# Kernel optimization log

Hardware: AMD Instinct MI355X
Metric: run time of the kernel (lower is better)

## Reference

```python
import jax, jax.numpy as jnp
import numpy as np

B, T, C = 4, 1024, 1024
N_HEAD = 16
MEMORY = 64  # sliding-window size: key j visible to query i iff 0 <= i-j <= MEMORY


def setup_inputs() -> dict:
    key = jax.random.key(0)
    k1, k2, k3 = jax.random.split(key, 3)
    x = jax.random.normal(k1, (B, T, C), dtype=jnp.float32)
    # torch Linear weight is [out, in]; we store transposed [in, out] for x @ W
    W_attn = jax.random.normal(k2, (C, 3 * C), dtype=jnp.float32) * (1.0 / np.sqrt(C))
    W_proj = jax.random.normal(k3, (C, C), dtype=jnp.float32) * (1.0 / np.sqrt(C))
    return {"x": x, "W_attn": W_attn, "W_proj": W_proj}


def reference(x, W_attn, W_proj):
    Bv, Tv, Cv = x.shape
    hd = Cv // N_HEAD
    qkv = x @ W_attn                               # [B,T,3C]
    q, k, v = jnp.split(qkv, 3, axis=-1)
    def heads(t):
        return t.reshape(Bv, Tv, N_HEAD, hd).transpose(0, 2, 1, 3)  # [B,H,T,hd]
    q, k, v = heads(q), heads(k), heads(v)
    scale = 1.0 / np.sqrt(hd)
    scores = jnp.einsum('bhqd,bhkd->bhqk', q, k) * scale            # [B,H,T,T]
    i = jnp.arange(Tv)
    diff = i[:, None] - i[None, :]                                  # i - j
    band_mask = (diff >= 0) & (diff <= MEMORY)                      # M1 * ~M2
    y = jax.nn.softmax(jnp.where(band_mask, scores, -jnp.inf), axis=-1) @ v
    # get_att=True path: full causal attention probabilities (no window)
    att = jax.nn.softmax(jnp.where(diff >= 0, scores, -jnp.inf), axis=-1)
    att_std = jnp.std(att, axis=0, ddof=1)                          # torch .std default ddof=1
    y = y.transpose(0, 2, 1, 3).reshape(Bv, Tv, Cv)
    y = y @ W_proj
    return (y, att, att_std)
```

## Files before the change

### kernel.cpp

```cpp
#include <hip/hip_runtime.h>
#include <hip/hip_bf16.h>
#include <stdint.h>

#define Bb 4
#define Tt 1024
#define Hh 16
#define HD 64
#define C3 3072
#define WIN 64

typedef __bf16 bf16x8 __attribute__((ext_vector_type(8)));
typedef float f32x4 __attribute__((ext_vector_type(4)));

#define MFMA16(a, b, c) __builtin_amdgcn_mfma_f32_16x16x32_bf16((a), (b), (c), 0, 0, 0)

static __device__ __forceinline__ unsigned short f2bf(float f) {
  union { float f; unsigned u; } v; v.f = f;
  unsigned r = (v.u + 0x7FFFu + ((v.u >> 16) & 1u)) >> 16;
  return (unsigned short)r;
}
static __device__ __forceinline__ float bf2f(unsigned short h) {
  union { unsigned u; float f; } v; v.u = ((unsigned)h) << 16;
  return v.f;
}

__global__ __launch_bounds__(256) void k_prep(const float* __restrict__ x,
                                              const float* __restrict__ Wa,
                                              const float* __restrict__ Wp,
                                              unsigned short* __restrict__ xbf,
                                              unsigned short* __restrict__ WtA,
                                              unsigned short* __restrict__ WtP) {
  __shared__ float tile[32][33];
  const int blk = blockIdx.x;
  const int tid = threadIdx.x;
  if (blk < 4096) {
    int i = blk * 256 + tid;
    float4 v = ((const float4*)x)[i];
    ushort4 o;
    o.x = f2bf(v.x); o.y = f2bf(v.y); o.z = f2bf(v.z); o.w = f2bf(v.w);
    ((ushort4*)xbf)[i] = o;
    return;
  }
  const float* Win; unsigned short* Wt; int N, n0, k0;
  if (blk < 7168) { int bb = blk - 4096; Win = Wa; Wt = WtA; N = 3072; n0 = (bb % 96) * 32; k0 = (bb / 96) * 32; }
  else           { int bb = blk - 7168; Win = Wp; Wt = WtP; N = 1024; n0 = (bb % 32) * 32; k0 = (bb / 32) * 32; }
  const int K = 1024;
  int tx = tid & 31, ty = tid >> 5;
  for (int r = ty; r < 32; r += 8)
    tile[r][tx] = Win[(size_t)(k0 + r) * N + n0 + tx];
  __syncthreads();
  for (int r = ty; r < 32; r += 8)
    Wt[(size_t)(n0 + r) * K + k0 + tx] = f2bf(tile[tx][r]);
}

template <int BF16_OUT, int SCALEQ>
__global__ __launch_bounds__(256) void k_gemm_bt(const unsigned short* __restrict__ A,
                                                 const unsigned short* __restrict__ Bt,
                                                 void* __restrict__ Cv, int M, int N, int K) {
  __shared__ unsigned short lds[2 * 128 * 32];
  unsigned short* as_ = lds;
  unsigned short* bs_ = lds + 128 * 32;
  const int tid = threadIdx.x;
  const int m0 = blockIdx.x * 128, n0 = blockIdx.y * 128;
  const int w = tid >> 6, lane = tid & 63;
  const int wm = (w >> 1) * 64, wn = (w & 1) * 64;
  const int lrow = lane & 15, lk = lane >> 4;

  f32x4 z = {0.f, 0.f, 0.f, 0.f};
  f32x4 acc[4][4];
#pragma unroll
  for (int i = 0; i < 4; ++i)
#pragma unroll
    for (int j = 0; j < 4; ++j) acc[i][j] = z;

  const int nk = K >> 5;
  for (int kt = 0; kt < nk; ++kt) {
    const int k0 = kt << 5;
    __syncthreads();
#pragma unroll
    for (int p = 0; p < 2; ++p) {
      int seg = tid + p * 256;
      int row = seg >> 2, ks = (seg & 3) << 3;
      __builtin_amdgcn_global_load_lds(
          (__attribute__((address_space(1))) void*)(A + (size_t)(m0 + row) * K + k0 + ks),
          (__attribute__((address_space(3))) void*)(as_ + seg * 8), 16, 0, 0);
      __builtin_amdgcn_global_load_lds(
          (__attribute__((address_space(1))) void*)(Bt + (size_t)(n0 + row) * K + k0 + ks),
          (__attribute__((address_space(3))) void*)(bs_ + seg * 8), 16, 0, 0);
    }
    __syncthreads();
    bf16x8 af[4], bfr[4];
#pragma unroll
    for (int f = 0; f < 4; ++f) {
      af[f] = *(const bf16x8*)(as_ + (wm + f * 16 + lrow) * 32 + lk * 8);
      bfr[f] = *(const bf16x8*)(bs_ + (wn + f * 16 + lrow) * 32 + lk * 8);
    }
#pragma unroll
    for (int i = 0; i < 4; ++i)
#pragma unroll
      for (int j = 0; j < 4; ++j) acc[i][j] = MFMA16(af[i], bfr[j], acc[i][j]);
  }
  const int r0 = lk * 4;
#pragma unroll
  for (int i = 0; i < 4; ++i)
#pragma unroll
    for (int j = 0; j < 4; ++j)
#pragma unroll
      for (int r = 0; r < 4; ++r) {
        int gm = m0 + wm + i * 16 + r0 + r;
        int gn = n0 + wn + j * 16 + lrow;
        float v = acc[i][j][r];
        if (SCALEQ) {
          if (gn < 1024) v *= 0.125f;
        }
        if (BF16_OUT)
          ((unsigned short*)Cv)[(size_t)gm * N + gn] = f2bf(v);
        else
          ((float*)Cv)[(size_t)gm * N + gn] = v;
      }
}

__global__ __launch_bounds__(256) void k_att(const unsigned short* __restrict__ qkv,
                                             float* __restrict__ att, float* __restrict__ astd) {
  const int ti = 31 - blockIdx.x;
  const int h = blockIdx.y;
  const int i0 = ti * 32;
  const int tid = threadIdx.x;
  const int w = tid >> 6, lane = tid & 63;
  const int lrow = lane & 15, lk = lane >> 4;

  __shared__ float smr[4][32][2];
  __shared__ float wbuf[4][32][36];

  {
    const int b1 = w;
    const size_t qb_ = ((size_t)(b1 * Tt + i0 + lrow)) * C3 + h * 64 + lk * 8;
    bf16x8 q00 = *(const bf16x8*)(qkv + qb_);
    bf16x8 q01 = *(const bf16x8*)(qkv + qb_ + 32);
    bf16x8 q10 = *(const bf16x8*)(qkv + qb_ + (size_t)16 * C3);
    bf16x8 q11 = *(const bf16x8*)(qkv + qb_ + (size_t)16 * C3 + 32);

    float m[2][4], l[2][4];
#pragma unroll
    for (int i2 = 0; i2 < 2; ++i2)
#pragma unroll
      for (int r = 0; r < 4; ++r) { m[i2][r] = -1e30f; l[i2][r] = 0.f; }

    for (int jt = 0; jt <= ti; ++jt) {
      const int j0 = jt * 32;
      const size_t krowa = ((size_t)(b1 * Tt + j0 + lrow)) * C3 + 1024 + h * 64 + lk * 8;
      const size_t krowb = krowa + (size_t)16 * C3;
      bf16x8 k00 = *(const bf16x8*)(qkv + krowa);
      bf16x8 k01 = *(const bf16x8*)(qkv + krowa + 32);
      bf16x8 k10 = *(const bf16x8*)(qkv + krowb);
      bf16x8 k11 = *(const bf16x8*)(qkv + krowb + 32);
      const int ja = j0 + lrow, jb2 = j0 + 16 + lrow;
#pragma unroll
      for (int i2 = 0; i2 < 2; ++i2) {
        bf16x8 qa = i2 ? q10 : q00;
        bf16x8 qb = i2 ? q11 : q01;
        f32x4 sa = {0.f, 0.f, 0.f, 0.f}, sb = {0.f, 0.f, 0.f, 0.f};
        sa = MFMA16(qa, k00, sa);
        sa = MFMA16(qb, k01, sa);
        sb = MFMA16(qa, k10, sb);
        sb = MFMA16(qb, k11, sb);
#pragma unroll
        for (int r = 0; r < 4; ++r) {
          int ig = i0 + i2 * 16 + lk * 4 + r;
          int oka = (ja <= ig), okb = (jb2 <= ig);
          float va = oka ? sa[r] : -1e30f;
          float vb = okb ? sb[r] : -1e30f;
          float mn = fmaxf(m[i2][r], fmaxf(va, vb));
          float pa = oka ? __expf(sa[r] - mn) : 0.f;
          float pb = okb ? __expf(sb[r] - mn) : 0.f;
          l[i2][r] = l[i2][r] * __expf(m[i2][r] - mn) + pa + pb;
          m[i2][r] = mn;
        }
      }
    }
#pragma unroll
    for (int i2 = 0; i2 < 2; ++i2)
#pragma unroll
      for (int r = 0; r < 4; ++r) {
        float mm = m[i2][r], ll = l[i2][r];
#pragma unroll
        for (int d = 1; d <= 8; d <<= 1) {
          float mo = __shfl_xor(mm, d);
          float lo = __shfl_xor(ll, d);
          float mn = fmaxf(mm, mo);
          ll = ll * __expf(mm - mn) + lo * __expf(mo - mn);
          mm = mn;
        }
        if (lrow == 0) {
          int row = i2 * 16 + lk * 4 + r;
          smr[b1][row][0] = mm;
          smr[b1][row][1] = 1.0f / ll;
        }
      }
  }
  __syncthreads();

  bf16x8 qf[4][2][2];
#pragma unroll
  for (int b = 0; b < 4; ++b) {
    const size_t qb_ = ((size_t)(b * Tt + i0 + lrow)) * C3 + h * 64 + lk * 8;
    qf[b][0][0] = *(const bf16x8*)(qkv + qb_);
    qf[b][0][1] = *(const bf16x8*)(qkv + qb_ + 32);
    qf[b][1][0] = *(const bf16x8*)(qkv + qb_ + (size_t)16 * C3);
    qf[b][1][1] = *(const bf16x8*)(qkv + qb_ + (size_t)16 * C3 + 32);
  }

  const float4 z4 = make_float4(0.f, 0.f, 0.f, 0.f);
  for (int jt = w; jt < 32; jt += 4) {
    const int j0 = jt * 32;
    if (jt > ti) {
#pragma unroll
      for (int b = 0; b < 4; ++b)
#pragma unroll
        for (int q = 0; q < 4; ++q) {
          int f = q * 64 + lane;
          int row = f >> 3, c4 = f & 7;
          *(float4*)&att[(((size_t)(b * Hh + h)) * Tt + i0 + row) * Tt + j0 + c4 * 4] = z4;
        }
#pragma unroll
      for (int q = 0; q < 4; ++q) {
        int f = q * 64 + lane;
        int row = f >> 3, c4 = f & 7;
        *(float4*)&astd[((size_t)h * Tt + i0 + row) * Tt + j0 + c4 * 4] = z4;
      }
      continue;
    }
    float s1[2][2][4], s2[2][2][4];
#pragma unroll
    for (int i2 = 0; i2 < 2; ++i2)
#pragma unroll
      for (int j2 = 0; j2 < 2; ++j2)
#pragma unroll
        for (int r = 0; r < 4; ++r) { s1[i2][j2][r] = 0.f; s2[i2][j2][r] = 0.f; }

#pragma unroll
    for (int b = 0; b < 4; ++b) {
      const size_t krowa = ((size_t)(b * Tt + j0 + lrow)) * C3 + 1024 + h * 64 + lk * 8;
      const size_t krowb = krowa + (size_t)16 * C3;
      bf16x8 k00 = *(const bf16x8*)(qkv + krowa);
      bf16x8 k01 = *(const bf16x8*)(qkv + krowa + 32);
      bf16x8 k10 = *(const bf16x8*)(qkv + krowb);
      bf16x8 k11 = *(const bf16x8*)(qkv + krowb + 32);
#pragma unroll
      for (int i2 = 0; i2 < 2; ++i2) {
        float mm[4], rr[4];
#pragma unroll
        for (int r = 0; r < 4; ++r) {
          int row = i2 * 16 + lk * 4 + r;
          mm[r] = smr[b][row][0];
          rr[r] = smr[b][row][1];
        }
#pragma unroll
        for (int j2 = 0; j2 < 2; ++j2) {
          f32x4 s = {0.f, 0.f, 0.f, 0.f};
          s = MFMA16(qf[b][i2][0], j2 ? k10 : k00, s);
          s = MFMA16(qf[b][i2][1], j2 ? k11 : k01, s);
          const int jg = j0 + j2 * 16 + lrow;
#pragma unroll
          for (int r = 0; r < 4; ++r) {
            int ig = i0 + i2 * 16 + lk * 4 + r;
            float p = (jg <= ig) ? __expf(s[r] - mm[r]) * rr[r] : 0.f;
            wbuf[w][i2 * 16 + lk * 4 + r][j2 * 16 + lrow] = p;
            s1[i2][j2][r] += p;
            s2[i2][j2][r] += p * p;
          }
        }
      }
#pragma unroll
      for (int q = 0; q < 4; ++q) {
        int f = q * 64 + lane;
        int row = f >> 3, c4 = f & 7;
        float4 v = *(float4*)&wbuf[w][row][c4 * 4];
        *(float4*)&att[(((size_t)(b * Hh + h)) * Tt + i0 + row) * Tt + j0 + c4 * 4] = v;
      }
    }
#pragma unroll
    for (int i2 = 0; i2 < 2; ++i2)
#pragma unroll
      for (int j2 = 0; j2 < 2; ++j2)
#pragma unroll
        for (int r = 0; r < 4; ++r) {
          float mean = s1[i2][j2][r] * 0.25f;
          float var = (s2[i2][j2][r] - 4.f * mean * mean) * (1.f / 3.f);
          wbuf[w][i2 * 16 + lk * 4 + r][j2 * 16 + lrow] = sqrtf(fmaxf(var, 0.f));
        }
#pragma unroll
    for (int q = 0; q < 4; ++q) {
      int f = q * 64 + lane;
      int row = f >> 3, c4 = f & 7;
      float4 v = *(float4*)&wbuf[w][row][c4 * 4];
      *(float4*)&astd[((size_t)h * Tt + i0 + row) * Tt + j0 + c4 * 4] = v;
    }
  }
}

__global__ __launch_bounds__(256) void k_bandy(const unsigned short* __restrict__ qkv,
                                               unsigned short* __restrict__ yh) {
  __shared__ unsigned short qls[64 * 66];
  __shared__ unsigned short kls[128 * 66];
  __shared__ unsigned short vls[128 * 66];
  __shared__ float pls[4][80];

  int blk = blockIdx.x;
  int it = blk & 15, h = (blk >> 4) & 15, b = blk >> 8;
  int i0 = it * 64;
  int jb = i0 - 64;
  int tid = threadIdx.x;

  for (int r = tid; r < 320; r += 256) {
    unsigned short* dst;
    int grow, sel;
    if (r < 64) { dst = qls + r * 66; grow = i0 + r; sel = 0; }
    else if (r < 192) { dst = kls + (r - 64) * 66; grow = jb + (r - 64); sel = 1; }
    else { dst = vls + (r - 192) * 66; grow = jb + (r - 192); sel = 2; }
    if (grow < 0) {
      for (int t = 0; t < 32; ++t) ((unsigned*)dst)[t] = 0u;
    } else {
      const unsigned* src = (const unsigned*)(qkv + ((size_t)(b * Tt + grow)) * C3 + sel * 1024 + h * 64);
      for (int t = 0; t < 32; ++t) ((unsigned*)dst)[t] = src[t];
    }
  }
  __syncthreads();

  const int w = tid >> 6, lane = tid & 63;
  for (int rr = 0; rr < 16; ++rr) {
    const int i = i0 + (w << 4) + rr;
    const int io = i - i0;
    const int ja = i - 64 + lane;
    const unsigned* qrow = (const unsigned*)(qls + io * 66);
    const unsigned* krow = (const unsigned*)(kls + (size_t)(io + lane) * 66);
    const unsigned* kerow = (const unsigned*)(kls + (size_t)(io + 64) * 66);
    float sa = 0.f, se = 0.f;
#pragma unroll 8
    for (int t = 0; t < 32; ++t) {
      unsigned qq = qrow[t];
      float q0 = bf2f((unsigned short)qq), q1 = bf2f((unsigned short)(qq >> 16));
      unsigned kk = krow[t];
      sa = fmaf(q0, bf2f((unsigned short)kk), sa);
      sa = fmaf(q1, bf2f((unsigned short)(kk >> 16)), sa);
      unsigned ke = kerow[t];
      se = fmaf(q0, bf2f((unsigned short)ke), se);
      se = fmaf(q1, bf2f((unsigned short)(ke >> 16)), se);
    }
    if (ja < 0) sa = -1e30f;
    float m = sa;
    m = fmaxf(m, __shfl_xor(m, 1));
    m = fmaxf(m, __shfl_xor(m, 2));
    m = fmaxf(m, __shfl_xor(m, 4));
    m = fmaxf(m, __shfl_xor(m, 8));
    m = fmaxf(m, __shfl_xor(m, 16));
    m = fmaxf(m, __shfl_xor(m, 32));
    m = fmaxf(m, se);
    float pa = __expf(sa - m);
    float pe = __expf(se - m);
    float sum = pa;
    sum += __shfl_xor(sum, 1);
    sum += __shfl_xor(sum, 2);
    sum += __shfl_xor(sum, 4);
    sum += __shfl_xor(sum, 8);
    sum += __shfl_xor(sum, 16);
    sum += __shfl_xor(sum, 32);
    sum += pe;
    float rl = 1.0f / sum;
    pls[w][lane] = pa * rl;
    if (lane == 0) pls[w][64] = pe * rl;
    float y = 0.f;
#pragma unroll 4
    for (int t = 0; t <= 64; ++t)
      y = fmaf(pls[w][t], bf2f(vls[(size_t)(io + t) * 66 + lane]), y);
    yh[((size_t)(b * Tt + i)) * 1024 + h * 64 + lane] = f2bf(y);
  }
}

extern "C" void kernel_launch(void* const* d_in, const int* in_sizes, int n_in,
                              void* d_out, int out_size, void* d_ws, size_t ws_size,
                              hipStream_t stream) {
  const float* x = (const float*)d_in[0];
  const float* Wa = (const float*)d_in[1];
  const float* Wp = (const float*)d_in[2];

  float* out = (float*)d_out;
  float* y_out = out;
  float* att = out + (size_t)4194304;
  float* astd = out + (size_t)71303168;

  char* ws = (char*)d_ws;
  unsigned short* qkv = (unsigned short*)ws;
  unsigned short* yh = (unsigned short*)(ws + 25165824);
  unsigned short* WtP = (unsigned short*)(ws + 33554432);

  char* yreg = (char*)d_out;
  unsigned short* WtA = (unsigned short*)yreg;
  unsigned short* xbf = (unsigned short*)(yreg + 6291456);

  k_prep<<<8192, 256, 0, stream>>>(x, Wa, Wp, xbf, WtA, WtP);
  k_gemm_bt<1, 1><<<dim3(32, 24), 256, 0, stream>>>(xbf, WtA, qkv, 4096, 3072, 1024);
  k_att<<<dim3(32, 16), 256, 0, stream>>>(qkv, att, astd);
  k_bandy<<<1024, 256, 0, stream>>>(qkv, yh);
  k_gemm_bt<0, 0><<<dim3(32, 8), 256, 0, stream>>>(yh, WtP, y_out, 4096, 1024, 1024);
}
```

Baseline: 295.6 us.

## Split causal attention into stats, zero-fill, and tile-parallel probability kernels

The monolithic attention kernel is split into three kernels. A stats kernel computes the per-row softmax max and inverse sum and writes them to workspace. A zero kernel fills the upper-triangle regions of att and att_std. A 3D-grid kernel then computes each 32x32 lower-triangle tile independently, reading the stats from global memory. The aim is to spread the uneven causal work across many more blocks and to take zero-fill off the compute path, at the cost of extra launches, a global stats round trip, and many early-exit blocks.

```diff
diff --git a/kernel.cpp b/kernel.cpp
--- a/kernel.cpp
+++ b/kernel.cpp
@@ -120,85 +120,103 @@
       }
 }
 
-__global__ __launch_bounds__(256) void k_att(const unsigned short* __restrict__ qkv,
-                                             float* __restrict__ att, float* __restrict__ astd) {
-  const int ti = 31 - blockIdx.x;
+__global__ __launch_bounds__(256) void k_stats(const unsigned short* __restrict__ qkv,
+                                               float2* __restrict__ stats) {
+  int blk = blockIdx.x;
+  int it = blk & 15, h = (blk >> 4) & 15, b = blk >> 8;
+  int w = threadIdx.x >> 6, lane = threadIdx.x & 63;
+  int lrow = lane & 15, lk = lane >> 4;
+  int ibase = it * 64 + w * 16;
+
+  const size_t qrow = ((size_t)(b * Tt + ibase + lrow)) * C3 + h * 64 + lk * 8;
+  bf16x8 qf0 = *(const bf16x8*)(qkv + qrow);
+  bf16x8 qf1 = *(const bf16x8*)(qkv + qrow + 32);
+
+  float m[4] = {-1e30f, -1e30f, -1e30f, -1e30f};
+  float l[4] = {0.f, 0.f, 0.f, 0.f};
+  const int nt = (ibase + 15) >> 5;
+  for (int jt = 0; jt <= nt; ++jt) {
+    const int j0 = jt * 32;
+    const size_t krowa = ((size_t)(b * Tt + j0 + lrow)) * C3 + 1024 + h * 64 + lk * 8;
+    const size_t krowb = krowa + (size_t)16 * C3;
+    bf16x8 ka0 = *(const bf16x8*)(qkv + krowa);
+    bf16x8 ka1 = *(const bf16x8*)(qkv + krowa + 32);
+    bf16x8 kb0 = *(const bf16x8*)(qkv + krowb);
+    bf16x8 kb1 = *(const bf16x8*)(qkv + krowb + 32);
+    f32x4 sa = {0.f, 0.f, 0.f, 0.f}, sb = {0.f, 0.f, 0.f, 0.f};
+    sa = MFMA16(qf0, ka0, sa);
+    sa = MFMA16(qf1, ka1, sa);
+    sb = MFMA16(qf0, kb0, sb);
+    sb = MFMA16(qf1, kb1, sb);
+    const int ja = j0 + lrow, jb2 = j0 + 16 + lrow;
+#pragma unroll
+    for (int r = 0; r < 4; ++r) {
+      int ig = ibase + lk * 4 + r;
+      int oka = (ja <= ig), okb = (jb2 <= ig);
+      float va = oka ? sa[r] : -1e30f;
+      float vb = okb ? sb[r] : -1e30f;
+      float mn = fmaxf(m[r], fmaxf(va, vb));
+      float pa = oka ? __expf(sa[r] - mn) : 0.f;
+      float pb = okb ? __expf(sb[r] - mn) : 0.f;
+      l[r] = l[r] * __expf(m[r] - mn) + pa + pb;
+      m[r] = mn;
+    }
+  }
+#pragma unroll
+  for (int r = 0; r < 4; ++r) {
+    float mm = m[r], ll = l[r];
+#pragma unroll
+    for (int d = 1; d <= 8; d <<= 1) {
+      float mo = __shfl_xor(mm, d);
+      float lo = __shfl_xor(ll, d);
+      float mn = fmaxf(mm, mo);
+      ll = ll * __expf(mm - mn) + lo * __expf(mo - mn);
+      mm = mn;
+    }
+    if (lrow == 0) {
+      int ig = ibase + lk * 4 + r;
+      stats[((size_t)(b * Hh + h)) * Tt + ig] = make_float2(mm, 1.0f / ll);
+    }
+  }
+}
+
+__global__ __launch_bounds__(256) void k_zero(float* __restrict__ att, float* __restrict__ astd) {
+  const int ti = blockIdx.x;
   const int h = blockIdx.y;
+  const int i0 = ti * 32, c0 = (ti + 1) * 32;
+  const int nc4 = (Tt - c0) >> 2;
+  const int tid = threadIdx.x;
+  const float4 z4 = make_float4(0.f, 0.f, 0.f, 0.f);
+#pragma unroll
+  for (int row = 0; row < 32; ++row) {
+    float4* a0 = (float4*)&att[(((size_t)(0 * Hh + h)) * Tt + i0 + row) * Tt + c0];
+    float4* a1 = (float4*)&att[(((size_t)(1 * Hh + h)) * Tt + i0 + row) * Tt + c0];
+    float4* a2 = (float4*)&att[(((size_t)(2 * Hh + h)) * Tt + i0 + row) * Tt + c0];
+    float4* a3 = (float4*)&att[(((size_t)(3 * Hh + h)) * Tt + i0 + row) * Tt + c0];
+    float4* as = (float4*)&astd[((size_t)h * Tt + i0 + row) * Tt + c0];
+    for (int c = tid; c < nc4; c += 256) {
+      a0[c] = z4; a1[c] = z4; a2[c] = z4; a3[c] = z4; as[c] = z4;
+    }
+  }
+}
+
+__global__ __launch_bounds__(256) void k_att2(const unsigned short* __restrict__ qkv,
+                                              const float2* __restrict__ stats,
+                                              float* __restrict__ att, float* __restrict__ astd) {
+  const int jg = blockIdx.x;
+  const int ti = 31 - blockIdx.y;
+  if (jg * 4 > ti) return;
+  const int h = blockIdx.z;
   const int i0 = ti * 32;
   const int tid = threadIdx.x;
   const int w = tid >> 6, lane = tid & 63;
+  const int jt = jg * 4 + w;
   const int lrow = lane & 15, lk = lane >> 4;
 
-  __shared__ float smr[4][32][2];
   __shared__ float wbuf[4][32][36];
 
-  {
-    const int b1 = w;
-    const size_t qb_ = ((size_t)(b1 * Tt + i0 + lrow)) * C3 + h * 64 + lk * 8;
-    bf16x8 q00 = *(const bf16x8*)(qkv + qb_);
-    bf16x8 q01 = *(const bf16x8*)(qkv + qb_ + 32);
-    bf16x8 q10 = *(const bf16x8*)(qkv + qb_ + (size_t)16 * C3);
-    bf16x8 q11 = *(const bf16x8*)(qkv + qb_ + (size_t)16 * C3 + 32);
-
-    float m[2][4], l[2][4];
-#pragma unroll
-    for (int i2 = 0; i2 < 2; ++i2)
-#pragma unroll
-      for (int r = 0; r < 4; ++r) { m[i2][r] = -1e30f; l[i2][r] = 0.f; }
-
-    for (int jt = 0; jt <= ti; ++jt) {
-      const int j0 = jt * 32;
-      const size_t krowa = ((size_t)(b1 * Tt + j0 + lrow)) * C3 + 1024 + h * 64 + lk * 8;
-      const size_t krowb = krowa + (size_t)16 * C3;
-      bf16x8 k00 = *(const bf16x8*)(qkv + krowa);
-      bf16x8 k01 = *(const bf16x8*)(qkv + krowa + 32);
-      bf16x8 k10 = *(const bf16x8*)(qkv + krowb);
-      bf16x8 k11 = *(const bf16x8*)(qkv + krowb + 32);
-      const int ja = j0 + lrow, jb2 = j0 + 16 + lrow;
-#pragma unroll
-      for (int i2 = 0; i2 < 2; ++i2) {
-        bf16x8 qa = i2 ? q10 : q00;
-        bf16x8 qb = i2 ? q11 : q01;
-        f32x4 sa = {0.f, 0.f, 0.f, 0.f}, sb = {0.f, 0.f, 0.f, 0.f};
-        sa = MFMA16(qa, k00, sa);
-        sa = MFMA16(qb, k01, sa);
-        sb = MFMA16(qa, k10, sb);
-        sb = MFMA16(qb, k11, sb);
-#pragma unroll
-        for (int r = 0; r < 4; ++r) {
-          int ig = i0 + i2 * 16 + lk * 4 + r;
-          int oka = (ja <= ig), okb = (jb2 <= ig);
-          float va = oka ? sa[r] : -1e30f;
-          float vb = okb ? sb[r] : -1e30f;
-          float mn = fmaxf(m[i2][r], fmaxf(va, vb));
-          float pa = oka ? __expf(sa[r] - mn) : 0.f;
-          float pb = okb ? __expf(sb[r] - mn) : 0.f;
-          l[i2][r] = l[i2][r] * __expf(m[i2][r] - mn) + pa + pb;
-          m[i2][r] = mn;
-        }
-      }
-    }
-#pragma unroll
-    for (int i2 = 0; i2 < 2; ++i2)
-#pragma unroll
-      for (int r = 0; r < 4; ++r) {
-        float mm = m[i2][r], ll = l[i2][r];
-#pragma unroll
-        for (int d = 1; d <= 8; d <<= 1) {
-          float mo = __shfl_xor(mm, d);
-          float lo = __shfl_xor(ll, d);
-          float mn = fmaxf(mm, mo);
-          ll = ll * __expf(mm - mn) + lo * __expf(mo - mn);
-          mm = mn;
-        }
-        if (lrow == 0) {
-          int row = i2 * 16 + lk * 4 + r;
-          smr[b1][row][0] = mm;
-          smr[b1][row][1] = 1.0f / ll;
-        }
-      }
-  }
-  __syncthreads();
+  if (jt > ti) return;
+  const int j0 = jt * 32;
 
   bf16x8 qf[4][2][2];
 #pragma unroll
@@ -210,92 +228,70 @@
     qf[b][1][1] = *(const bf16x8*)(qkv + qb_ + (size_t)16 * C3 + 32);
   }
 
-  const float4 z4 = make_float4(0.f, 0.f, 0.f, 0.f);
-  for (int jt = w; jt < 32; jt += 4) {
-    const int j0 = jt * 32;
-    if (jt > ti) {
-#pragma unroll
-      for (int b = 0; b < 4; ++b)
-#pragma unroll
-        for (int q = 0; q < 4; ++q) {
-          int f = q * 64 + lane;
-          int row = f >> 3, c4 = f & 7;
-          *(float4*)&att[(((size_t)(b * Hh + h)) * Tt + i0 + row) * Tt + j0 + c4 * 4] = z4;
-        }
-#pragma unroll
-      for (int q = 0; q < 4; ++q) {
-        int f = q * 64 + lane;
-        int row = f >> 3, c4 = f & 7;
-        *(float4*)&astd[((size_t)h * Tt + i0 + row) * Tt + j0 + c4 * 4] = z4;
+  float s1[2][2][4], s2[2][2][4];
+#pragma unroll
+  for (int i2 = 0; i2 < 2; ++i2)
+#pragma unroll
+    for (int j2 = 0; j2 < 2; ++j2)
+#pragma unroll
+      for (int r = 0; r < 4; ++r) { s1[i2][j2][r] = 0.f; s2[i2][j2][r] = 0.f; }
+
+#pragma unroll
+  for (int b = 0; b < 4; ++b) {
+    const size_t krowa = ((size_t)(b * Tt + j0 + lrow)) * C3 + 1024 + h * 64 + lk * 8;
+    const size_t krowb = krowa + (size_t)16 * C3;
+    bf16x8 k00 = *(const bf16x8*)(qkv + krowa);
+    bf16x8 k01 = *(const bf16x8*)(qkv + krowa + 32);
+    bf16x8 k10 = *(const bf16x8*)(qkv + krowb);
+    bf16x8 k11 = *(const bf16x8*)(qkv + krowb + 32);
+#pragma unroll
+    for (int i2 = 0; i2 < 2; ++i2) {
+      float mm[4], rr[4];
+#pragma unroll
+      for (int r = 0; r < 4; ++r) {
+        float2 st = stats[((size_t)(b * Hh + h)) * Tt + i0 + i2 * 16 + lk * 4 + r];
+        mm[r] = st.x; rr[r] = st.y;
       }
-      continue;
-    }
-    float s1[2][2][4], s2[2][2][4];
-#pragma unroll
-    for (int i2 = 0; i2 < 2; ++i2)
-#pragma unroll
-      for (int j2 = 0; j2 < 2; ++j2)
-#pragma unroll
-        for (int r = 0; r < 4; ++r) { s1[i2][j2][r] = 0.f; s2[i2][j2][r] = 0.f; }
-
-#pragma unroll
-    for (int b = 0; b < 4; ++b) {
-      const size_t krowa = ((size_t)(b * Tt + j0 + lrow)) * C3 + 1024 + h * 64 + lk * 8;
-      const size_t krowb = krowa + (size_t)16 * C3;
-      bf16x8 k00 = *(const bf16x8*)(qkv + krowa);
-      bf16x8 k01 = *(const bf16x8*)(qkv + krowa + 32);
-      bf16x8 k10 = *(const bf16x8*)(qkv + krowb);
-      bf16x8 k11 = *(const bf16x8*)(qkv + krowb + 32);
-#pragma unroll
-      for (int i2 = 0; i2 < 2; ++i2) {
-        float mm[4], rr[4];
+#pragma unroll
+      for (int j2 = 0; j2 < 2; ++j2) {
+        f32x4 s = {0.f, 0.f, 0.f, 0.f};
+        s = MFMA16(qf[b][i2][0], j2 ? k10 : k00, s);
+        s = MFMA16(qf[b][i2][1], j2 ? k11 : k01, s);
+        const int jg2 = j0 + j2 * 16 + lrow;
 #pragma unroll
         for (int r = 0; r < 4; ++r) {
-          int row = i2 * 16 + lk * 4 + r;
-          mm[r] = smr[b][row][0];
-          rr[r] = smr[b][row][1];
-        }
-#pragma unroll
-        for (int j2 = 0; j2 < 2; ++j2) {
-          f32x4 s = {0.f, 0.f, 0.f, 0.f};
-          s = MFMA16(qf[b][i2][0], j2 ? k10 : k00, s);
-          s = MFMA16(qf[b][i2][1], j2 ? k11 : k01, s);
-          const int jg = j0 + j2 * 16 + lrow;
-#pragma unroll
-          for (int r = 0; r < 4; ++r) {
-            int ig = i0 + i2 * 16 + lk * 4 + r;
-            float p = (jg <= ig) ? __expf(s[r] - mm[r]) * rr[r] : 0.f;
-            wbuf[w][i2 * 16 + lk * 4 + r][j2 * 16 + lrow] = p;
-            s1[i2][j2][r] += p;
-            s2[i2][j2][r] += p * p;
-          }
+          int ig = i0 + i2 * 16 + lk * 4 + r;
+          float p = (jg2 <= ig) ? __expf(s[r] - mm[r]) * rr[r] : 0.f;
+          wbuf[w][i2 * 16 + lk * 4 + r][j2 * 16 + lrow] = p;
+          s1[i2][j2][r] += p;
+          s2[i2][j2][r] += p * p;
         }
       }
-#pragma unroll
-      for (int q = 0; q < 4; ++q) {
-        int f = q * 64 + lane;
-        int row = f >> 3, c4 = f & 7;
-        float4 v = *(float4*)&wbuf[w][row][c4 * 4];
-        *(float4*)&att[(((size_t)(b * Hh + h)) * Tt + i0 + row) * Tt + j0 + c4 * 4] = v;
-      }
-    }
-#pragma unroll
-    for (int i2 = 0; i2 < 2; ++i2)
-#pragma unroll
-      for (int j2 = 0; j2 < 2; ++j2)
-#pragma unroll
-        for (int r = 0; r < 4; ++r) {
-          float mean = s1[i2][j2][r] * 0.25f;
-          float var = (s2[i2][j2][r] - 4.f * mean * mean) * (1.f / 3.f);
-          wbuf[w][i2 * 16 + lk * 4 + r][j2 * 16 + lrow] = sqrtf(fmaxf(var, 0.f));
-        }
+    }
 #pragma unroll
     for (int q = 0; q < 4; ++q) {
       int f = q * 64 + lane;
       int row = f >> 3, c4 = f & 7;
       float4 v = *(float4*)&wbuf[w][row][c4 * 4];
-      *(float4*)&astd[((size_t)h * Tt + i0 + row) * Tt + j0 + c4 * 4] = v;
-    }
+      *(float4*)&att[(((size_t)(b * Hh + h)) * Tt + i0 + row) * Tt + j0 + c4 * 4] = v;
+    }
+  }
+#pragma unroll
+  for (int i2 = 0; i2 < 2; ++i2)
+#pragma unroll
+    for (int j2 = 0; j2 < 2; ++j2)
+#pragma unroll
+      for (int r = 0; r < 4; ++r) {
+        float mean = s1[i2][j2][r] * 0.25f;
+        float var = (s2[i2][j2][r] - 4.f * mean * mean) * (1.f / 3.f);
+        wbuf[w][i2 * 16 + lk * 4 + r][j2 * 16 + lrow] = sqrtf(fmaxf(var, 0.f));
+      }
+#pragma unroll
+  for (int q = 0; q < 4; ++q) {
+    int f = q * 64 + lane;
+    int row = f >> 3, c4 = f & 7;
+    float4 v = *(float4*)&wbuf[w][row][c4 * 4];
+    *(float4*)&astd[((size_t)h * Tt + i0 + row) * Tt + j0 + c4 * 4] = v;
   }
 }
 
@@ -393,6 +389,7 @@
   unsigned short* qkv = (unsigned short*)ws;
   unsigned short* yh = (unsigned short*)(ws + 25165824);
   unsigned short* WtP = (unsigned short*)(ws + 33554432);
+  float2* stats = (float2*)(ws + 35651584);
 
   char* yreg = (char*)d_out;
   unsigned short* WtA = (unsigned short*)yreg;
@@ -400,7 +397,9 @@
 
   k_prep<<<8192, 256, 0, stream>>>(x, Wa, Wp, xbf, WtA, WtP);
   k_gemm_bt<1, 1><<<dim3(32, 24), 256, 0, stream>>>(xbf, WtA, qkv, 4096, 3072, 1024);
-  k_att<<<dim3(32, 16), 256, 0, stream>>>(qkv, att, astd);
+  k_stats<<<1024, 256, 0, stream>>>(qkv, stats);
+  k_zero<<<dim3(31, 16), 256, 0, stream>>>(att, astd);
+  k_att2<<<dim3(8, 32, 16), 256, 0, stream>>>(qkv, stats, att, astd);
   k_bandy<<<1024, 256, 0, stream>>>(qkv, yh);
   k_gemm_bt<0, 0><<<dim3(32, 8), 256, 0, stream>>>(yh, WtP, y_out, 4096, 1024, 1024);
 }
```

Result: slower. 369.7 us (+25.1%).
